# Kernel optimization log

Hardware: AMD Instinct MI355X
Metric: run time of the kernel (lower is better)

## Reference

```python
import jax, jax.numpy as jnp
import numpy as np

GAMMA = 1.0
NUM_CLASSES = 128


def setup_inputs() -> dict:
    key = jax.random.key(0)
    k1, k2, k3 = jax.random.split(key, 3)
    B, D, P = 8192, 512, 4096
    feature = jax.random.normal(k1, (B, D), dtype=jnp.float32)
    label = jax.random.randint(k2, (B,), 0, NUM_CLASSES)
    proto_features = jax.random.normal(k3, (P, D), dtype=jnp.float32)
    proto_labels = jnp.arange(P) % NUM_CLASSES  # every class has prototypes
    return {"feature": feature, "label": label,
            "proto_features": proto_features, "proto_labels": proto_labels}


def reference(feature, label, proto_features, proto_labels):
    # squared euclidean distances [B, P] via ||f||^2 + ||p||^2 - 2 f.p
    f_sq = jnp.sum(feature * feature, axis=-1, keepdims=True)          # [B,1]
    p_sq = jnp.sum(proto_features * proto_features, axis=-1)           # [P]
    d2 = f_sq + p_sq[None, :] - 2.0 * (feature @ proto_features.T)      # [B,P]
    d2 = jnp.maximum(d2, 0.0)
    logits = -GAMMA * d2                                                # [B,P]
    # denominator: sum over ALL prototypes; numerator: sum over own-class protos
    log_den = jax.scipy.special.logsumexp(logits, axis=-1)              # [B]
    same = proto_labels[None, :] == label[:, None]                      # [B,P]
    neg_inf = jnp.finfo(logits.dtype).min
    log_num = jax.scipy.special.logsumexp(
        jnp.where(same, logits, neg_inf), axis=-1)                      # [B]
    # loss = -log(num/den) per sample
    return log_den - log_num
```

## Files before the change

kernel.cpp:

```cpp
#include <hip/hip_runtime.h>
#include <hip/hip_bf16.h>

#define BN 8192
#define DK 512
#define PN 4096
#define GY 8
#define PPB 512
#define CH 16
#define NCH 32
#define STRIDE 520
#define BUFELE (CH * STRIDE)
#define SENT (-1.0e30f)
#define L2E 1.4426950408889634f
#define LN2 0.6931471805599453f

typedef __bf16 bf16x8 __attribute__((ext_vector_type(8)));
typedef __bf16 bf16x4 __attribute__((ext_vector_type(4)));
typedef float f32x4 __attribute__((ext_vector_type(4)));

__device__ __forceinline__ float ex2(float x) { return __builtin_amdgcn_exp2f(x); }

__device__ __forceinline__ void gl_lds16(const void* g, void* l) {
    __builtin_amdgcn_global_load_lds(
        (const __attribute__((address_space(1))) void*)g,
        (__attribute__((address_space(3))) void*)l, 16, 0, 0);
}

__global__ __launch_bounds__(256) void k_prep(const float* __restrict__ proto,
                                              __bf16* __restrict__ pB,
                                              float* __restrict__ p_sq) {
    int p  = blockIdx.x * 4 + (threadIdx.x >> 6);
    int ln = threadIdx.x & 63;
    const float* src = proto + (size_t)p * DK;
    float4 a = *(const float4*)(src + ln * 4);
    float4 b = *(const float4*)(src + 256 + ln * 4);
    float s = a.x * a.x + a.y * a.y + a.z * a.z + a.w * a.w
            + b.x * b.x + b.y * b.y + b.z * b.z + b.w * b.w;
#pragma unroll
    for (int m = 1; m < 64; m <<= 1) s += __shfl_xor(s, m, 64);
    int sidx = (p & 127) * 32 + (p >> 7);
    bf16x4 c0, c1;
    c0[0] = (__bf16)a.x; c0[1] = (__bf16)a.y; c0[2] = (__bf16)a.z; c0[3] = (__bf16)a.w;
    c1[0] = (__bf16)b.x; c1[1] = (__bf16)b.y; c1[2] = (__bf16)b.z; c1[3] = (__bf16)b.w;
    *(bf16x4*)(pB + (size_t)sidx * DK + ln * 4) = c0;
    *(bf16x4*)(pB + (size_t)sidx * DK + 256 + ln * 4) = c1;
    if (ln == 0) p_sq[sidx] = s * L2E;
}

__global__ __launch_bounds__(256, 2) void k_main(
        const float* __restrict__ feat,
        const __bf16* __restrict__ pB,
        const float* __restrict__ p_sq,
        const int* __restrict__ label,
        float4* __restrict__ part) {

    __shared__ __bf16 sM[4 * BUFELE];
    __shared__ float  sPsq[PPB];

    const int t    = threadIdx.x;
    const int w    = t >> 6;
    const int l    = t & 63;
    const int ln   = l & 15;
    const int quad = l >> 4;
    const int bx   = blockIdx.x;
    const int gy   = blockIdx.y;
    const int rw   = bx * 128 + w * 32;
    const int p0   = gy * PPB;

    int lab[2][4];
#pragma unroll
    for (int mf = 0; mf < 2; ++mf)
#pragma unroll
        for (int r = 0; r < 4; ++r)
            lab[mf][r] = label[rw + mf * 16 + quad * 4 + r];

#define ISSUE(c) {                                                          \
        const __bf16* g = pB + (size_t)(p0 + (c) * CH + w * 4) * DK + l * 8; \
        __bf16* lp = sM + ((c) & 3) * BUFELE + (w * 4) * STRIDE;            \
        _Pragma("unroll")                                                   \
        for (int j = 0; j < 4; ++j)                                         \
            gl_lds16(g + j * DK, lp + j * STRIDE);                          \
    }

    ISSUE(0);
    sPsq[t]       = p_sq[p0 + t];
    sPsq[t + 256] = p_sq[p0 + t + 256];

    __bf16* sA = sM + 2 * BUFELE;
    bf16x8 afrag[2][16];
#pragma unroll 1
    for (int q = 0; q < 4; ++q) {
#pragma unroll 4
        for (int i = 0; i < 16; ++i) {
            int idx = t + 256 * i;
            int row = idx >> 7;
            int c4  = idx & 127;
            float4 v = *(const float4*)(feat + (size_t)(bx * 128 + q * 32 + row) * DK + c4 * 4);
            bf16x4 cv;
            cv[0] = (__bf16)v.x; cv[1] = (__bf16)v.y; cv[2] = (__bf16)v.z; cv[3] = (__bf16)v.w;
            *(bf16x4*)(sA + row * STRIDE + c4 * 4) = cv;
        }
        __syncthreads();
        if (w == q) {
#pragma unroll
            for (int mf = 0; mf < 2; ++mf)
#pragma unroll
                for (int ks = 0; ks < 16; ++ks)
                    afrag[mf][ks] = *(const bf16x8*)(sA + (mf * 16 + ln) * STRIDE + ks * 32 + quad * 8);
        }
        __syncthreads();
    }

    ISSUE(1);
    ISSUE(2);

    float Md[2][4], Sd[2][4], Mn[2][4], Sn[2][4], zp[2][4];
#pragma unroll
    for (int mf = 0; mf < 2; ++mf)
#pragma unroll
        for (int r = 0; r < 4; ++r) {
            Md[mf][r] = SENT; Sd[mf][r] = 0.f;
            Mn[mf][r] = SENT; Sn[mf][r] = 0.f;
            zp[mf][r] = SENT;
        }
    int clsp = -1;

#define DEN_SLICE(j) {                                                      \
        const int mfj = (j) >> 2, rj = (j) & 3;                             \
        float z  = zp[mfj][rj];                                             \
        float nm = fmaxf(Md[mfj][rj], z);                                   \
        Sd[mfj][rj] = fmaf(Sd[mfj][rj], ex2(Md[mfj][rj] - nm), ex2(z - nm)); \
        Md[mfj][rj] = nm; }

#define NUM_MERGE() {                                                       \
        int anyhit = 0;                                                     \
        _Pragma("unroll")                                                   \
        for (int mf = 0; mf < 2; ++mf)                                      \
        { _Pragma("unroll")                                                 \
          for (int r = 0; r < 4; ++r) anyhit |= (clsp == lab[mf][r]); }     \
        if (__any(anyhit)) {                                                \
            _Pragma("unroll")                                               \
            for (int mf = 0; mf < 2; ++mf)                                  \
            { _Pragma("unroll")                                             \
              for (int r = 0; r < 4; ++r) {                                 \
                bool hit = (clsp == lab[mf][r]);                            \
                float z  = zp[mf][r];                                       \
                float nm = fmaxf(Mn[mf][r], z);                             \
                float sn = fmaf(Sn[mf][r], ex2(Mn[mf][r] - nm), ex2(z - nm)); \
                Mn[mf][r] = hit ? nm : Mn[mf][r];                           \
                Sn[mf][r] = hit ? sn : Sn[mf][r];                           \
            } } } }

#define COMPUTE(nt) {                                                       \
        const __bf16* sB = sM + ((nt) & 3) * BUFELE;                        \
        float nps = -sPsq[(nt) * CH + ln];                                  \
        f32x4 a0 = (f32x4){0.f, 0.f, 0.f, 0.f};                             \
        f32x4 a1 = (f32x4){0.f, 0.f, 0.f, 0.f};                             \
        _Pragma("unroll")                                                   \
        for (int ks = 0; ks < 16; ++ks) {                                   \
            bf16x8 b = *(const bf16x8*)(sB + ln * STRIDE + ks * 32 + quad * 8); \
            a0 = __builtin_amdgcn_mfma_f32_16x16x32_bf16(afrag[0][ks], b, a0, 0, 0, 0); \
            a1 = __builtin_amdgcn_mfma_f32_16x16x32_bf16(afrag[1][ks], b, a1, 0, 0, 0); \
            if ((ks & 1) == 0) DEN_SLICE(ks >> 1);                          \
        }                                                                   \
        NUM_MERGE();                                                        \
        _Pragma("unroll")                                                   \
        for (int r = 0; r < 4; ++r) {                                       \
            zp[0][r] = fmaf(a0[r], 2.0f * L2E, nps);                        \
            zp[1][r] = fmaf(a1[r], 2.0f * L2E, nps);                        \
        }                                                                   \
        clsp = gy * 16 + ((nt) >> 1); }

#pragma unroll 1
    for (int nt = 0; nt < NCH - 2; ++nt) {
        asm volatile("s_waitcnt vmcnt(8)" ::: "memory");
        __builtin_amdgcn_s_barrier();
        if (nt + 3 < NCH) ISSUE(nt + 3);
        COMPUTE(nt);
    }
    asm volatile("s_waitcnt vmcnt(4)" ::: "memory");
    __builtin_amdgcn_s_barrier();
    COMPUTE(NCH - 2);
    asm volatile("s_waitcnt vmcnt(0)" ::: "memory");
    __builtin_amdgcn_s_barrier();
    COMPUTE(NCH - 1);

#pragma unroll
    for (int j = 0; j < 8; ++j) DEN_SLICE(j);
    NUM_MERGE();

#undef COMPUTE
#undef DEN_SLICE
#undef NUM_MERGE
#undef ISSUE

#pragma unroll
    for (int mf = 0; mf < 2; ++mf)
#pragma unroll
        for (int r = 0; r < 4; ++r) {
            float md = Md[mf][r], sd = Sd[mf][r];
            float mn = Mn[mf][r], sn = Sn[mf][r];
#pragma unroll
            for (int m = 1; m < 16; m <<= 1) {
                float omd = __shfl_xor(md, m, 64);
                float osd = __shfl_xor(sd, m, 64);
                float omn = __shfl_xor(mn, m, 64);
                float osn = __shfl_xor(sn, m, 64);
                float nm = fmaxf(md, omd);
                sd = sd * ex2(md - nm) + osd * ex2(omd - nm);
                md = nm;
                nm = fmaxf(mn, omn);
                sn = sn * ex2(mn - nm) + osn * ex2(omn - nm);
                mn = nm;
            }
            if (ln == 0) {
                int row = rw + mf * 16 + quad * 4 + r;
                part[row * GY + gy] = make_float4(md, sd, mn, sn);
            }
        }
}

__global__ __launch_bounds__(256) void k_comb(const float4* __restrict__ part,
                                              float* __restrict__ out) {
    int row = blockIdx.x * 256 + threadIdx.x;
    float md = SENT, sd = 0.f, mn = SENT, sn = 0.f;
#pragma unroll
    for (int q = 0; q < GY; ++q) {
        float4 v = part[row * GY + q];
        float nm = fmaxf(md, v.x);
        sd = sd * ex2(md - nm) + v.y * ex2(v.x - nm);
        md = nm;
        nm = fmaxf(mn, v.z);
        sn = sn * ex2(mn - nm) + v.w * ex2(v.z - nm);
        mn = nm;
    }
    out[row] = ((md + __builtin_amdgcn_logf(sd)) - (mn + __builtin_amdgcn_logf(sn))) * LN2;
}

extern "C" void kernel_launch(void* const* d_in, const int* in_sizes, int n_in,
                              void* d_out, int out_size, void* d_ws, size_t ws_size,
                              hipStream_t stream) {
    const float* feat   = (const float*)d_in[0];
    const int*   label  = (const int*)d_in[1];
    const float* proto  = (const float*)d_in[2];
    float*       out    = (float*)d_out;

    char* w = (char*)d_ws;
    __bf16* pB    = (__bf16*)(w);
    float*  p_sq  = (float*)(w + 4194304);
    float4* part  = (float4*)(w + 4243456);

    hipLaunchKernelGGL(k_prep, dim3(PN / 4), dim3(256), 0, stream,
                       proto, pB, p_sq);
    hipLaunchKernelGGL(k_main, dim3(64, GY), dim3(256), 0, stream,
                       feat, pB, p_sq, label, part);
    hipLaunchKernelGGL(k_comb, dim3(BN / 256), dim3(256), 0, stream,
                       part, out);
}
```

Measured before the change: 125.3 us.

## Split prototype range finer, double-buffer LDS, and parallelize combine reduction

The prototype dimension is split into 16 slices of 256 instead of 8 of 512, doubling the grid. LDS staging drops from four buffers to two, so four blocks fit per CU. The hand-tuned vmcnt pipeline becomes a simpler issue-next, compute, barrier loop with s_setprio raised around the MFMA section. The combine kernel now reduces each row's 16 partials with wavefront shuffles instead of a serial per-thread loop. The cost is that each block reloads and converts the fp32 features twice as often, and the shallower prefetch exposes more load latency.

```diff
diff --git a/kernel.cpp b/kernel.cpp
--- a/kernel.cpp
+++ b/kernel.cpp
@@ -4,10 +4,10 @@
 #define BN 8192
 #define DK 512
 #define PN 4096
-#define GY 8
-#define PPB 512
+#define GY 16
+#define PPB 256
 #define CH 16
-#define NCH 32
+#define NCH 16
 #define STRIDE 520
 #define BUFELE (CH * STRIDE)
 #define SENT (-1.0e30f)
@@ -47,14 +47,14 @@
     if (ln == 0) p_sq[sidx] = s * L2E;
 }
 
-__global__ __launch_bounds__(256, 2) void k_main(
+__global__ __launch_bounds__(256, 4) void k_main(
         const float* __restrict__ feat,
         const __bf16* __restrict__ pB,
         const float* __restrict__ p_sq,
         const int* __restrict__ label,
         float4* __restrict__ part) {
 
-    __shared__ __bf16 sM[4 * BUFELE];
+    __shared__ __bf16 sM[2 * BUFELE];
     __shared__ float  sPsq[PPB];
 
     const int t    = threadIdx.x;
@@ -74,19 +74,16 @@
         for (int r = 0; r < 4; ++r)
             lab[mf][r] = label[rw + mf * 16 + quad * 4 + r];
 
+    sPsq[t & 255] = p_sq[p0 + (t & 255)];
+
 #define ISSUE(c) {                                                          \
         const __bf16* g = pB + (size_t)(p0 + (c) * CH + w * 4) * DK + l * 8; \
-        __bf16* lp = sM + ((c) & 3) * BUFELE + (w * 4) * STRIDE;            \
+        __bf16* lp = sM + ((c) & 1) * BUFELE + (w * 4) * STRIDE;            \
         _Pragma("unroll")                                                   \
         for (int j = 0; j < 4; ++j)                                         \
             gl_lds16(g + j * DK, lp + j * STRIDE);                          \
     }
 
-    ISSUE(0);
-    sPsq[t]       = p_sq[p0 + t];
-    sPsq[t + 256] = p_sq[p0 + t + 256];
-
-    __bf16* sA = sM + 2 * BUFELE;
     bf16x8 afrag[2][16];
 #pragma unroll 1
     for (int q = 0; q < 4; ++q) {
@@ -98,7 +95,7 @@
             float4 v = *(const float4*)(feat + (size_t)(bx * 128 + q * 32 + row) * DK + c4 * 4);
             bf16x4 cv;
             cv[0] = (__bf16)v.x; cv[1] = (__bf16)v.y; cv[2] = (__bf16)v.z; cv[3] = (__bf16)v.w;
-            *(bf16x4*)(sA + row * STRIDE + c4 * 4) = cv;
+            *(bf16x4*)(sM + row * STRIDE + c4 * 4) = cv;
         }
         __syncthreads();
         if (w == q) {
@@ -106,13 +103,13 @@
             for (int mf = 0; mf < 2; ++mf)
 #pragma unroll
                 for (int ks = 0; ks < 16; ++ks)
-                    afrag[mf][ks] = *(const bf16x8*)(sA + (mf * 16 + ln) * STRIDE + ks * 32 + quad * 8);
+                    afrag[mf][ks] = *(const bf16x8*)(sM + (mf * 16 + ln) * STRIDE + ks * 32 + quad * 8);
         }
         __syncthreads();
     }
 
-    ISSUE(1);
-    ISSUE(2);
+    ISSUE(0);
+    __syncthreads();
 
     float Md[2][4], Sd[2][4], Mn[2][4], Sn[2][4], zp[2][4];
 #pragma unroll
@@ -151,45 +148,40 @@
                 Sn[mf][r] = hit ? sn : Sn[mf][r];                           \
             } } } }
 
-#define COMPUTE(nt) {                                                       \
-        const __bf16* sB = sM + ((nt) & 3) * BUFELE;                        \
-        float nps = -sPsq[(nt) * CH + ln];                                  \
-        f32x4 a0 = (f32x4){0.f, 0.f, 0.f, 0.f};                             \
-        f32x4 a1 = (f32x4){0.f, 0.f, 0.f, 0.f};                             \
-        _Pragma("unroll")                                                   \
-        for (int ks = 0; ks < 16; ++ks) {                                   \
-            bf16x8 b = *(const bf16x8*)(sB + ln * STRIDE + ks * 32 + quad * 8); \
-            a0 = __builtin_amdgcn_mfma_f32_16x16x32_bf16(afrag[0][ks], b, a0, 0, 0, 0); \
-            a1 = __builtin_amdgcn_mfma_f32_16x16x32_bf16(afrag[1][ks], b, a1, 0, 0, 0); \
-            if ((ks & 1) == 0) DEN_SLICE(ks >> 1);                          \
-        }                                                                   \
-        NUM_MERGE();                                                        \
-        _Pragma("unroll")                                                   \
-        for (int r = 0; r < 4; ++r) {                                       \
-            zp[0][r] = fmaf(a0[r], 2.0f * L2E, nps);                        \
-            zp[1][r] = fmaf(a1[r], 2.0f * L2E, nps);                        \
-        }                                                                   \
-        clsp = gy * 16 + ((nt) >> 1); }
-
 #pragma unroll 1
-    for (int nt = 0; nt < NCH - 2; ++nt) {
-        asm volatile("s_waitcnt vmcnt(8)" ::: "memory");
-        __builtin_amdgcn_s_barrier();
-        if (nt + 3 < NCH) ISSUE(nt + 3);
-        COMPUTE(nt);
-    }
-    asm volatile("s_waitcnt vmcnt(4)" ::: "memory");
-    __builtin_amdgcn_s_barrier();
-    COMPUTE(NCH - 2);
-    asm volatile("s_waitcnt vmcnt(0)" ::: "memory");
-    __builtin_amdgcn_s_barrier();
-    COMPUTE(NCH - 1);
+    for (int nt = 0; nt < NCH; ++nt) {
+        if (nt + 1 < NCH) ISSUE(nt + 1);
+
+        const __bf16* sB = sM + (nt & 1) * BUFELE;
+        float nps = -sPsq[nt * CH + ln];
+        f32x4 a0 = (f32x4){0.f, 0.f, 0.f, 0.f};
+        f32x4 a1 = (f32x4){0.f, 0.f, 0.f, 0.f};
+
+        __builtin_amdgcn_s_setprio(1);
+#pragma unroll
+        for (int ks = 0; ks < 16; ++ks) {
+            bf16x8 b = *(const bf16x8*)(sB + ln * STRIDE + ks * 32 + quad * 8);
+            a0 = __builtin_amdgcn_mfma_f32_16x16x32_bf16(afrag[0][ks], b, a0, 0, 0, 0);
+            a1 = __builtin_amdgcn_mfma_f32_16x16x32_bf16(afrag[1][ks], b, a1, 0, 0, 0);
+            if ((ks & 1) == 0) DEN_SLICE(ks >> 1);
+        }
+        __builtin_amdgcn_s_setprio(0);
+
+        NUM_MERGE();
+#pragma unroll
+        for (int r = 0; r < 4; ++r) {
+            zp[0][r] = fmaf(a0[r], 2.0f * L2E, nps);
+            zp[1][r] = fmaf(a1[r], 2.0f * L2E, nps);
+        }
+        clsp = gy * 8 + (nt >> 1);
+
+        __syncthreads();
+    }
 
 #pragma unroll
     for (int j = 0; j < 8; ++j) DEN_SLICE(j);
     NUM_MERGE();
 
-#undef COMPUTE
 #undef DEN_SLICE
 #undef NUM_MERGE
 #undef ISSUE
@@ -222,19 +214,28 @@
 
 __global__ __launch_bounds__(256) void k_comb(const float4* __restrict__ part,
                                               float* __restrict__ out) {
-    int row = blockIdx.x * 256 + threadIdx.x;
-    float md = SENT, sd = 0.f, mn = SENT, sn = 0.f;
-#pragma unroll
-    for (int q = 0; q < GY; ++q) {
-        float4 v = part[row * GY + q];
-        float nm = fmaxf(md, v.x);
-        sd = sd * ex2(md - nm) + v.y * ex2(v.x - nm);
+    int t   = threadIdx.x;
+    int w   = t >> 6;
+    int l   = t & 63;
+    int row = blockIdx.x * 16 + w * 4 + (l >> 4);
+    int q   = l & 15;
+    float4 v = part[row * GY + q];
+    float md = v.x, sd = v.y, mn = v.z, sn = v.w;
+#pragma unroll
+    for (int m = 1; m < 16; m <<= 1) {
+        float omd = __shfl_xor(md, m, 64);
+        float osd = __shfl_xor(sd, m, 64);
+        float omn = __shfl_xor(mn, m, 64);
+        float osn = __shfl_xor(sn, m, 64);
+        float nm = fmaxf(md, omd);
+        sd = sd * ex2(md - nm) + osd * ex2(omd - nm);
         md = nm;
-        nm = fmaxf(mn, v.z);
-        sn = sn * ex2(mn - nm) + v.w * ex2(v.z - nm);
+        nm = fmaxf(mn, omn);
+        sn = sn * ex2(mn - nm) + osn * ex2(omn - nm);
         mn = nm;
     }
-    out[row] = ((md + __builtin_amdgcn_logf(sd)) - (mn + __builtin_amdgcn_logf(sn))) * LN2;
+    if (q == 0)
+        out[row] = ((md + __builtin_amdgcn_logf(sd)) - (mn + __builtin_amdgcn_logf(sn))) * LN2;
 }
 
 extern "C" void kernel_launch(void* const* d_in, const int* in_sizes, int n_in,
@@ -252,8 +253,8 @@
 
     hipLaunchKernelGGL(k_prep, dim3(PN / 4), dim3(256), 0, stream,
                        proto, pB, p_sq);
-    hipLaunchKernelGGL(k_main, dim3(64, GY), dim3(256), 0, stream,
+    hipLaunchKernelGGL(k_main, dim3(BN / 128, GY), dim3(256), 0, stream,
                        feat, pB, p_sq, label, part);
-    hipLaunchKernelGGL(k_comb, dim3(BN / 256), dim3(256), 0, stream,
+    hipLaunchKernelGGL(k_comb, dim3(BN / 16), dim3(256), 0, stream,
                        part, out);
 }
```

New measurement: 270.6 us. +116.0%, slower.
